# Kernel optimization log

Measured on AMD Instinct MI355X. Metric: run time of the kernel, lower is better.

The kernel has to match this reference:

```python
import jax, jax.numpy as jnp
import numpy as np

N = 20000
E = 320000
IN_F = 256
HEADS = 4
OUT_F = 64
NEG_SLOPE = 0.2


def setup_inputs() -> dict:
    key = jax.random.key(0)
    k1, k2, k3, k4 = jax.random.split(key, 4)
    x = jax.random.normal(k1, (N, IN_F), dtype=jnp.float32)
    edge_index = jax.random.randint(k2, (2, E), 0, N, dtype=jnp.int64)
    # Linear W: [in_features, heads*out_features] (xavier-ish scale)
    W = jax.random.normal(k3, (IN_F, HEADS * OUT_F), dtype=jnp.float32) * (1.0 / np.sqrt(IN_F))
    # attention vector: [1, heads, 2*out_features]
    att = jax.random.normal(k4, (1, HEADS, 2 * OUT_F), dtype=jnp.float32) * 0.1
    b = jnp.zeros((HEADS * OUT_F,), dtype=jnp.float32)
    return {"x": x, "W": W, "att": att, "b": b, "edge_index": edge_index}


def _leaky_relu(v):
    return jnp.where(v > 0, v, NEG_SLOPE * v)


def reference(x, W, att, b, edge_index):
    n = x.shape[0]
    heads = att.shape[1]
    d = att.shape[2] // 2

    # add self loops: edge_index -> [2, E+N]
    loops = jnp.arange(n, dtype=edge_index.dtype)
    src = jnp.concatenate([edge_index[0], loops])
    dst = jnp.concatenate([edge_index[1], loops])

    # projected node features [N, heads, out]
    h = (x @ W).reshape(n, heads, d)

    # attention scores: leaky_relu is elementwise, so the concat-then-dot
    # splits into src/dst halves of `att` -> avoids materializing h_cat.
    a_src = att[0, :, :d]  # [heads, out]
    a_dst = att[0, :, d:]  # [heads, out]
    h_src = h[src]  # [Etot, heads, out]
    scores = (
        jnp.einsum("ehd,hd->eh", _leaky_relu(h_src), a_src)
        + jnp.einsum("ehd,hd->eh", _leaky_relu(h[dst]), a_dst)
    )  # [Etot, heads]

    # NOTE: original module applies softmax over ALL edges (dim=0), not per-dst
    w = jax.nn.softmax(scores, axis=0)  # [Etot, heads]

    # scatter-aggregate weighted src features into dst nodes
    out = jax.ops.segment_sum(h_src * w[:, :, None], dst, num_segments=n)  # [N, heads, out]

    return out.reshape(n, heads * d) + b
```

## Files before the change

kernel.cpp:

```cpp
#include <hip/hip_runtime.h>

#define NN 20000
#define EE 320000
#define TE 340000
#define NEG 0.2f
#define NB_SCORE 1329
#define NB_GEMM 625
#define CAP 96

typedef __attribute__((ext_vector_type(8))) _Float16 half8;
typedef __attribute__((ext_vector_type(4))) _Float16 half4v;
typedef __attribute__((ext_vector_type(4))) float f32x4;

__device__ __forceinline__ float lrelu(float v) { return v > 0.f ? v : NEG * v; }

__global__ __launch_bounds__(256) void k_wsplit(const float* __restrict__ W,
                                                _Float16* __restrict__ Wh, _Float16* __restrict__ Wl) {
    int c = blockIdx.x;
    int k = threadIdx.x;
    float w = W[k * 256 + c];
    _Float16 hi = (_Float16)w;
    _Float16 lo = (_Float16)(w - (float)hi);
    int idx = (k >> 3) * 2048 + c * 8 + (k & 7);
    Wh[idx] = hi;
    Wl[idx] = lo;
}

__global__ __launch_bounds__(256, 4) void k_gemm(const float* __restrict__ x,
                                                 const _Float16* __restrict__ Wh,
                                                 const _Float16* __restrict__ Wl,
                                                 const float* __restrict__ att, _Float16* __restrict__ h16,
                                                 float* __restrict__ Es, float* __restrict__ Ed,
                                                 int* __restrict__ cnt) {
    __shared__ _Float16 xh[32][264];
    __shared__ _Float16 xl[32][264];
    const int tid = threadIdx.x;
    const int r0 = blockIdx.x * 32;

    if (tid < 32) cnt[r0 + tid] = 0;

    const float4* x4 = (const float4*)x;
    #pragma unroll
    for (int i = 0; i < 8; ++i) {
        int slot = tid + i * 256;
        int row = slot >> 6, c4 = slot & 63;
        float4 v = x4[(r0 + row) * 64 + c4];
        _Float16 h0 = (_Float16)v.x, h1 = (_Float16)v.y, h2 = (_Float16)v.z, h3 = (_Float16)v.w;
        half4v hv = {h0, h1, h2, h3};
        half4v lv = {(_Float16)(v.x - (float)h0), (_Float16)(v.y - (float)h1),
                     (_Float16)(v.z - (float)h2), (_Float16)(v.w - (float)h3)};
        *(half4v*)&xh[row][c4 * 4] = hv;
        *(half4v*)&xl[row][c4 * 4] = lv;
    }
    __syncthreads();

    const int lane = tid & 63, wid = tid >> 6;
    const int ch = wid;
    const int grp = lane >> 4, li = lane & 15;

    f32x4 acc[2][4];
    #pragma unroll
    for (int rt = 0; rt < 2; ++rt)
        #pragma unroll
        for (int i = 0; i < 4; ++i) acc[rt][i] = (f32x4){0.f, 0.f, 0.f, 0.f};

    const _Float16* bb_h = Wh + (ch * 64 + li) * 8 + grp * 2048;
    const _Float16* bb_l = Wl + (ch * 64 + li) * 8 + grp * 2048;

    for (int ks = 0; ks < 8; ++ks) {
        half8 ah0 = *(const half8*)&xh[li][ks * 32 + grp * 8];
        half8 al0 = *(const half8*)&xl[li][ks * 32 + grp * 8];
        half8 ah1 = *(const half8*)&xh[16 + li][ks * 32 + grp * 8];
        half8 al1 = *(const half8*)&xl[16 + li][ks * 32 + grp * 8];
        const _Float16* ph = bb_h + ks * 8192;
        const _Float16* pl = bb_l + ks * 8192;
        #pragma unroll
        for (int ct = 0; ct < 4; ++ct) {
            half8 bh = *(const half8*)(ph + ct * 128);
            half8 bl = *(const half8*)(pl + ct * 128);
            acc[0][ct] = __builtin_amdgcn_mfma_f32_16x16x32_f16(ah0, bh, acc[0][ct], 0, 0, 0);
            acc[0][ct] = __builtin_amdgcn_mfma_f32_16x16x32_f16(al0, bh, acc[0][ct], 0, 0, 0);
            acc[0][ct] = __builtin_amdgcn_mfma_f32_16x16x32_f16(ah0, bl, acc[0][ct], 0, 0, 0);
            acc[0][ct] = __builtin_amdgcn_mfma_f32_16x16x32_f16(al0, bl, acc[0][ct], 0, 0, 0);
            acc[1][ct] = __builtin_amdgcn_mfma_f32_16x16x32_f16(ah1, bh, acc[1][ct], 0, 0, 0);
            acc[1][ct] = __builtin_amdgcn_mfma_f32_16x16x32_f16(al1, bh, acc[1][ct], 0, 0, 0);
            acc[1][ct] = __builtin_amdgcn_mfma_f32_16x16x32_f16(ah1, bl, acc[1][ct], 0, 0, 0);
            acc[1][ct] = __builtin_amdgcn_mfma_f32_16x16x32_f16(al1, bl, acc[1][ct], 0, 0, 0);
        }
    }

    float pss[2][4] = {{0.f,0.f,0.f,0.f},{0.f,0.f,0.f,0.f}};
    float psd[2][4] = {{0.f,0.f,0.f,0.f},{0.f,0.f,0.f,0.f}};
    #pragma unroll
    for (int rt = 0; rt < 2; ++rt) {
        #pragma unroll
        for (int ct = 0; ct < 4; ++ct) {
            int cl = ct * 16 + li;
            float avc = att[ch * 128 + cl];
            float dvc = att[ch * 128 + 64 + cl];
            #pragma unroll
            for (int reg = 0; reg < 4; ++reg) {
                float v = acc[rt][ct][reg];
                h16[(r0 + rt * 16 + grp * 4 + reg) * 256 + ch * 64 + cl] = (_Float16)v;
                float l = lrelu(v);
                pss[rt][reg] += l * avc;
                psd[rt][reg] += l * dvc;
            }
        }
    }
    #pragma unroll
    for (int rt = 0; rt < 2; ++rt)
        #pragma unroll
        for (int reg = 0; reg < 4; ++reg) {
            #pragma unroll
            for (int m = 1; m < 16; m <<= 1) {
                pss[rt][reg] += __shfl_xor(pss[rt][reg], m, 64);
                psd[rt][reg] += __shfl_xor(psd[rt][reg], m, 64);
            }
        }
    if (li == 0) {
        #pragma unroll
        for (int rt = 0; rt < 2; ++rt)
            #pragma unroll
            for (int reg = 0; reg < 4; ++reg) {
                int row = r0 + rt * 16 + grp * 4 + reg;
                Es[row * 4 + ch] = expf(pss[rt][reg]);
                Ed[row * 4 + ch] = expf(psd[rt][reg]);
            }
    }
}

__global__ __launch_bounds__(256) void k_fill(const int* __restrict__ es, const int* __restrict__ ed,
                                              const float* __restrict__ Es, const float* __restrict__ Ed,
                                              int* __restrict__ cnt, int* __restrict__ bucket,
                                              float4* __restrict__ psum) {
    __shared__ float4 ls[4];
    int e = blockIdx.x * 256 + threadIdx.x;
    int tid = threadIdx.x, lane = tid & 63, wid = tid >> 6;
    float4 p = {0.f, 0.f, 0.f, 0.f};
    if (e < TE) {
        int si = e < EE ? es[e] : e - EE;
        int di = e < EE ? ed[e] : e - EE;
        int pos = atomicAdd(cnt + di, 1);
        if (pos < CAP) bucket[di * CAP + pos] = si;
        float4 a = ((const float4*)Es)[si];
        float4 d = ((const float4*)Ed)[di];
        p.x = a.x * d.x; p.y = a.y * d.y; p.z = a.z * d.z; p.w = a.w * d.w;
    }
    #pragma unroll
    for (int m = 32; m > 0; m >>= 1) {
        p.x += __shfl_xor(p.x, m, 64);
        p.y += __shfl_xor(p.y, m, 64);
        p.z += __shfl_xor(p.z, m, 64);
        p.w += __shfl_xor(p.w, m, 64);
    }
    if (lane == 0) ls[wid] = p;
    __syncthreads();
    if (tid == 0) {
        float4 t;
        t.x = ls[0].x + ls[1].x + ls[2].x + ls[3].x;
        t.y = ls[0].y + ls[1].y + ls[2].y + ls[3].y;
        t.z = ls[0].z + ls[1].z + ls[2].z + ls[3].z;
        t.w = ls[0].w + ls[1].w + ls[2].w + ls[3].w;
        psum[blockIdx.x] = t;
    }
}

__global__ __launch_bounds__(256) void k_comb(const float4* __restrict__ psum, float* __restrict__ hstat) {
    __shared__ float4 zred[4];
    int tid = threadIdx.x, lane = tid & 63, wid = tid >> 6;
    float4 z = {0.f, 0.f, 0.f, 0.f};
    for (int i = tid; i < NB_SCORE; i += 256) {
        float4 s = psum[i];
        z.x += s.x; z.y += s.y; z.z += s.z; z.w += s.w;
    }
    #pragma unroll
    for (int m = 32; m > 0; m >>= 1) {
        z.x += __shfl_xor(z.x, m, 64);
        z.y += __shfl_xor(z.y, m, 64);
        z.z += __shfl_xor(z.z, m, 64);
        z.w += __shfl_xor(z.w, m, 64);
    }
    if (lane == 0) zred[wid] = z;
    __syncthreads();
    if (tid == 0) {
        float4 t;
        t.x = zred[0].x + zred[1].x + zred[2].x + zred[3].x;
        t.y = zred[0].y + zred[1].y + zred[2].y + zred[3].y;
        t.z = zred[0].z + zred[1].z + zred[2].z + zred[3].z;
        t.w = zred[0].w + zred[1].w + zred[2].w + zred[3].w;
        hstat[0] = 1.0f / t.x; hstat[1] = 1.0f / t.y;
        hstat[2] = 1.0f / t.z; hstat[3] = 1.0f / t.w;
    }
}

__global__ __launch_bounds__(256) void k_gather(const int* __restrict__ cnt, const int* __restrict__ bucket,
                                                const float* __restrict__ Es, const float* __restrict__ Ed,
                                                const _Float16* __restrict__ h16, const float* __restrict__ b,
                                                const float* __restrict__ hstat, float* __restrict__ out) {
    int n = blockIdx.x * 4 + (threadIdx.x >> 6);
    int lane = threadIdx.x & 63;
    int head = lane >> 4;
    int len = cnt[n]; len = len < CAP ? len : CAP;
    const int* bsi = bucket + n * CAP;
    const half4v* h4 = (const half4v*)h16;
    float4 a0 = {0.f, 0.f, 0.f, 0.f}, a1 = a0, a2 = a0, a3 = a0;
    int j = 0;
    for (; j + 7 < len; j += 8) {
        int s0 = bsi[j],     s1 = bsi[j + 1], s2 = bsi[j + 2], s3 = bsi[j + 3];
        int s4 = bsi[j + 4], s5 = bsi[j + 5], s6 = bsi[j + 6], s7 = bsi[j + 7];
        float w0 = Es[s0 * 4 + head], w1 = Es[s1 * 4 + head];
        float w2 = Es[s2 * 4 + head], w3 = Es[s3 * 4 + head];
        float w4 = Es[s4 * 4 + head], w5 = Es[s5 * 4 + head];
        float w6 = Es[s6 * 4 + head], w7 = Es[s7 * 4 + head];
        half4v v0 = h4[s0 * 64 + lane], v1 = h4[s1 * 64 + lane];
        half4v v2 = h4[s2 * 64 + lane], v3 = h4[s3 * 64 + lane];
        half4v v4 = h4[s4 * 64 + lane], v5 = h4[s5 * 64 + lane];
        half4v v6 = h4[s6 * 64 + lane], v7 = h4[s7 * 64 + lane];
        a0.x += w0 * (float)v0.x; a0.y += w0 * (float)v0.y; a0.z += w0 * (float)v0.z; a0.w += w0 * (float)v0.w;
        a1.x += w1 * (float)v1.x; a1.y += w1 * (float)v1.y; a1.z += w1 * (float)v1.z; a1.w += w1 * (float)v1.w;
        a2.x += w2 * (float)v2.x; a2.y += w2 * (float)v2.y; a2.z += w2 * (float)v2.z; a2.w += w2 * (float)v2.w;
        a3.x += w3 * (float)v3.x; a3.y += w3 * (float)v3.y; a3.z += w3 * (float)v3.z; a3.w += w3 * (float)v3.w;
        a0.x += w4 * (float)v4.x; a0.y += w4 * (float)v4.y; a0.z += w4 * (float)v4.z; a0.w += w4 * (float)v4.w;
        a1.x += w5 * (float)v5.x; a1.y += w5 * (float)v5.y; a1.z += w5 * (float)v5.z; a1.w += w5 * (float)v5.w;
        a2.x += w6 * (float)v6.x; a2.y += w6 * (float)v6.y; a2.z += w6 * (float)v6.z; a2.w += w6 * (float)v6.w;
        a3.x += w7 * (float)v7.x; a3.y += w7 * (float)v7.y; a3.z += w7 * (float)v7.z; a3.w += w7 * (float)v7.w;
    }
    for (; j + 3 < len; j += 4) {
        int s0 = bsi[j], s1 = bsi[j + 1], s2 = bsi[j + 2], s3 = bsi[j + 3];
        float w0 = Es[s0 * 4 + head], w1 = Es[s1 * 4 + head];
        float w2 = Es[s2 * 4 + head], w3 = Es[s3 * 4 + head];
        half4v v0 = h4[s0 * 64 + lane], v1 = h4[s1 * 64 + lane];
        half4v v2 = h4[s2 * 64 + lane], v3 = h4[s3 * 64 + lane];
        a0.x += w0 * (float)v0.x; a0.y += w0 * (float)v0.y; a0.z += w0 * (float)v0.z; a0.w += w0 * (float)v0.w;
        a1.x += w1 * (float)v1.x; a1.y += w1 * (float)v1.y; a1.z += w1 * (float)v1.z; a1.w += w1 * (float)v1.w;
        a2.x += w2 * (float)v2.x; a2.y += w2 * (float)v2.y; a2.z += w2 * (float)v2.z; a2.w += w2 * (float)v2.w;
        a3.x += w3 * (float)v3.x; a3.y += w3 * (float)v3.y; a3.z += w3 * (float)v3.z; a3.w += w3 * (float)v3.w;
    }
    for (; j < len; ++j) {
        int s = bsi[j];
        float w = Es[s * 4 + head];
        half4v hv = h4[s * 64 + lane];
        a0.x += w * (float)hv.x; a0.y += w * (float)hv.y; a0.z += w * (float)hv.z; a0.w += w * (float)hv.w;
    }
    float scale = hstat[head] * Ed[n * 4 + head];
    float4 bb = ((const float4*)b)[lane];
    float4 o;
    o.x = bb.x + scale * (a0.x + a1.x + a2.x + a3.x);
    o.y = bb.y + scale * (a0.y + a1.y + a2.y + a3.y);
    o.z = bb.z + scale * (a0.z + a1.z + a2.z + a3.z);
    o.w = bb.w + scale * (a0.w + a1.w + a2.w + a3.w);
    ((float4*)out)[n * 64 + lane] = o;
}

extern "C" void kernel_launch(void* const* d_in, const int* in_sizes, int n_in,
                              void* d_out, int out_size, void* d_ws, size_t ws_size,
                              hipStream_t stream) {
    const float* x   = (const float*)d_in[0];
    const float* W   = (const float*)d_in[1];
    const float* att = (const float*)d_in[2];
    const float* b   = (const float*)d_in[3];
    const int*  eidx = (const int*)d_in[4];
    const int* es = eidx;
    const int* ed = eidx + EE;
    float* out = (float*)d_out;

    float* ws = (float*)d_ws;
    _Float16* h16 = (_Float16*)ws;
    float* Es     = (float*)(h16 + NN * 256);
    float* Ed     = Es + NN * 4;
    int*   cnt    = (int*)(Ed + NN * 4);
    int*   bucket = cnt + NN;
    float4* psum  = (float4*)(bucket + NN * CAP);
    float* hstat  = (float*)(psum + NB_SCORE + 1);
    _Float16* Wh  = (_Float16*)(hstat + 16);
    _Float16* Wl  = Wh + 256 * 256;

    k_wsplit<<<256, 256, 0, stream>>>(W, Wh, Wl);
    k_gemm  <<<NB_GEMM, 256, 0, stream>>>(x, Wh, Wl, att, h16, Es, Ed, cnt);
    k_fill  <<<NB_SCORE, 256, 0, stream>>>(es, ed, Es, Ed, cnt, bucket, psum);
    k_comb  <<<1, 256, 0, stream>>>(psum, hstat);
    k_gather<<<NN / 4, 256, 0, stream>>>(cnt, bucket, Es, Ed, h16, b, hstat, out);
}
```

Baseline: 86.42 us.

## Fuse softmax-normalizer reduction into fill via last-block pattern, shrink bucket indices

Removes the separate single-block combine kernel. The last fill block, found through an atomic done-counter that k_wsplit resets, now sums the per-block partial sums and writes the inverse normalizers. Bucket source indices are stored as 16-bit values, halving bucket traffic in fill and gather, and gather gains a 16-wide unrolled loop for more memory-level parallelism. This saves one kernel launch but adds atomics and fences, and the 16-bit indices only work because N is below 65536.

```diff
diff --git a/kernel.cpp b/kernel.cpp
--- a/kernel.cpp
+++ b/kernel.cpp
@@ -15,7 +15,9 @@
 __device__ __forceinline__ float lrelu(float v) { return v > 0.f ? v : NEG * v; }
 
 __global__ __launch_bounds__(256) void k_wsplit(const float* __restrict__ W,
-                                                _Float16* __restrict__ Wh, _Float16* __restrict__ Wl) {
+                                                _Float16* __restrict__ Wh, _Float16* __restrict__ Wl,
+                                                unsigned* __restrict__ done) {
+    if (blockIdx.x == 0 && threadIdx.x == 0) *done = 0u;
     int c = blockIdx.x;
     int k = threadIdx.x;
     float w = W[k * 256 + c];
@@ -132,9 +134,11 @@
 
 __global__ __launch_bounds__(256) void k_fill(const int* __restrict__ es, const int* __restrict__ ed,
                                               const float* __restrict__ Es, const float* __restrict__ Ed,
-                                              int* __restrict__ cnt, int* __restrict__ bucket,
-                                              float4* __restrict__ psum) {
+                                              int* __restrict__ cnt, unsigned short* __restrict__ bucket,
+                                              float* __restrict__ psumF, unsigned* __restrict__ done,
+                                              float* __restrict__ hstat) {
     __shared__ float4 ls[4];
+    __shared__ int amLast;
     int e = blockIdx.x * 256 + threadIdx.x;
     int tid = threadIdx.x, lane = tid & 63, wid = tid >> 6;
     float4 p = {0.f, 0.f, 0.f, 0.f};
@@ -142,7 +146,7 @@
         int si = e < EE ? es[e] : e - EE;
         int di = e < EE ? ed[e] : e - EE;
         int pos = atomicAdd(cnt + di, 1);
-        if (pos < CAP) bucket[di * CAP + pos] = si;
+        if (pos < CAP) bucket[di * CAP + pos] = (unsigned short)si;
         float4 a = ((const float4*)Es)[si];
         float4 d = ((const float4*)Ed)[di];
         p.x = a.x * d.x; p.y = a.y * d.y; p.z = a.z * d.z; p.w = a.w * d.w;
@@ -162,39 +166,48 @@
         t.y = ls[0].y + ls[1].y + ls[2].y + ls[3].y;
         t.z = ls[0].z + ls[1].z + ls[2].z + ls[3].z;
         t.w = ls[0].w + ls[1].w + ls[2].w + ls[3].w;
-        psum[blockIdx.x] = t;
-    }
-}
-
-__global__ __launch_bounds__(256) void k_comb(const float4* __restrict__ psum, float* __restrict__ hstat) {
-    __shared__ float4 zred[4];
-    int tid = threadIdx.x, lane = tid & 63, wid = tid >> 6;
-    float4 z = {0.f, 0.f, 0.f, 0.f};
-    for (int i = tid; i < NB_SCORE; i += 256) {
-        float4 s = psum[i];
-        z.x += s.x; z.y += s.y; z.z += s.z; z.w += s.w;
-    }
-    #pragma unroll
-    for (int m = 32; m > 0; m >>= 1) {
-        z.x += __shfl_xor(z.x, m, 64);
-        z.y += __shfl_xor(z.y, m, 64);
-        z.z += __shfl_xor(z.z, m, 64);
-        z.w += __shfl_xor(z.w, m, 64);
-    }
-    if (lane == 0) zred[wid] = z;
+        atomicExch(psumF + blockIdx.x * 4 + 0, t.x);
+        atomicExch(psumF + blockIdx.x * 4 + 1, t.y);
+        atomicExch(psumF + blockIdx.x * 4 + 2, t.z);
+        atomicExch(psumF + blockIdx.x * 4 + 3, t.w);
+        __threadfence();
+        unsigned v = atomicAdd(done, 1u);
+        amLast = (v == NB_SCORE - 1);
+    }
     __syncthreads();
-    if (tid == 0) {
-        float4 t;
-        t.x = zred[0].x + zred[1].x + zred[2].x + zred[3].x;
-        t.y = zred[0].y + zred[1].y + zred[2].y + zred[3].y;
-        t.z = zred[0].z + zred[1].z + zred[2].z + zred[3].z;
-        t.w = zred[0].w + zred[1].w + zred[2].w + zred[3].w;
-        hstat[0] = 1.0f / t.x; hstat[1] = 1.0f / t.y;
-        hstat[2] = 1.0f / t.z; hstat[3] = 1.0f / t.w;
-    }
-}
-
-__global__ __launch_bounds__(256) void k_gather(const int* __restrict__ cnt, const int* __restrict__ bucket,
+    if (amLast) {
+        __threadfence();
+        float4 z = {0.f, 0.f, 0.f, 0.f};
+        for (int i = tid; i < NB_SCORE; i += 256) {
+            z.x += atomicAdd(psumF + i * 4 + 0, 0.0f);
+            z.y += atomicAdd(psumF + i * 4 + 1, 0.0f);
+            z.z += atomicAdd(psumF + i * 4 + 2, 0.0f);
+            z.w += atomicAdd(psumF + i * 4 + 3, 0.0f);
+        }
+        #pragma unroll
+        for (int m = 32; m > 0; m >>= 1) {
+            z.x += __shfl_xor(z.x, m, 64);
+            z.y += __shfl_xor(z.y, m, 64);
+            z.z += __shfl_xor(z.z, m, 64);
+            z.w += __shfl_xor(z.w, m, 64);
+        }
+        __syncthreads();
+        if (lane == 0) ls[wid] = z;
+        __syncthreads();
+        if (tid == 0) {
+            float4 t;
+            t.x = ls[0].x + ls[1].x + ls[2].x + ls[3].x;
+            t.y = ls[0].y + ls[1].y + ls[2].y + ls[3].y;
+            t.z = ls[0].z + ls[1].z + ls[2].z + ls[3].z;
+            t.w = ls[0].w + ls[1].w + ls[2].w + ls[3].w;
+            hstat[0] = 1.0f / t.x; hstat[1] = 1.0f / t.y;
+            hstat[2] = 1.0f / t.z; hstat[3] = 1.0f / t.w;
+        }
+    }
+}
+
+__global__ __launch_bounds__(256) void k_gather(const int* __restrict__ cnt,
+                                                const unsigned short* __restrict__ bucket,
                                                 const float* __restrict__ Es, const float* __restrict__ Ed,
                                                 const _Float16* __restrict__ h16, const float* __restrict__ b,
                                                 const float* __restrict__ hstat, float* __restrict__ out) {
@@ -202,10 +215,32 @@
     int lane = threadIdx.x & 63;
     int head = lane >> 4;
     int len = cnt[n]; len = len < CAP ? len : CAP;
-    const int* bsi = bucket + n * CAP;
+    const unsigned short* bsi = bucket + n * CAP;
     const half4v* h4 = (const half4v*)h16;
     float4 a0 = {0.f, 0.f, 0.f, 0.f}, a1 = a0, a2 = a0, a3 = a0;
     int j = 0;
+    for (; j + 15 < len; j += 16) {
+        int s[16];
+        float w[16];
+        #pragma unroll
+        for (int q = 0; q < 16; ++q) s[q] = bsi[j + q];
+        #pragma unroll
+        for (int q = 0; q < 16; ++q) w[q] = Es[s[q] * 4 + head];
+        half4v v[16];
+        #pragma unroll
+        for (int q = 0; q < 16; ++q) v[q] = h4[s[q] * 64 + lane];
+        #pragma unroll
+        for (int q = 0; q < 16; q += 4) {
+            a0.x += w[q] * (float)v[q].x;     a0.y += w[q] * (float)v[q].y;
+            a0.z += w[q] * (float)v[q].z;     a0.w += w[q] * (float)v[q].w;
+            a1.x += w[q+1] * (float)v[q+1].x; a1.y += w[q+1] * (float)v[q+1].y;
+            a1.z += w[q+1] * (float)v[q+1].z; a1.w += w[q+1] * (float)v[q+1].w;
+            a2.x += w[q+2] * (float)v[q+2].x; a2.y += w[q+2] * (float)v[q+2].y;
+            a2.z += w[q+2] * (float)v[q+2].z; a2.w += w[q+2] * (float)v[q+2].w;
+            a3.x += w[q+3] * (float)v[q+3].x; a3.y += w[q+3] * (float)v[q+3].y;
+            a3.z += w[q+3] * (float)v[q+3].z; a3.w += w[q+3] * (float)v[q+3].w;
+        }
+    }
     for (; j + 7 < len; j += 8) {
         int s0 = bsi[j],     s1 = bsi[j + 1], s2 = bsi[j + 2], s3 = bsi[j + 3];
         int s4 = bsi[j + 4], s5 = bsi[j + 5], s6 = bsi[j + 6], s7 = bsi[j + 7];
@@ -270,15 +305,15 @@
     float* Es     = (float*)(h16 + NN * 256);
     float* Ed     = Es + NN * 4;
     int*   cnt    = (int*)(Ed + NN * 4);
-    int*   bucket = cnt + NN;
-    float4* psum  = (float4*)(bucket + NN * CAP);
-    float* hstat  = (float*)(psum + NB_SCORE + 1);
-    _Float16* Wh  = (_Float16*)(hstat + 16);
+    unsigned short* bucket = (unsigned short*)(cnt + NN);
+    float* psumF  = (float*)(bucket + NN * CAP);
+    unsigned* done = (unsigned*)(psumF + NB_SCORE * 4);
+    float* hstat  = (float*)(done + 3);
+    _Float16* Wh  = (_Float16*)(hstat + 12);
     _Float16* Wl  = Wh + 256 * 256;
 
-    k_wsplit<<<256, 256, 0, stream>>>(W, Wh, Wl);
+    k_wsplit<<<256, 256, 0, stream>>>(W, Wh, Wl, done);
     k_gemm  <<<NB_GEMM, 256, 0, stream>>>(x, Wh, Wl, att, h16, Es, Ed, cnt);
-    k_fill  <<<NB_SCORE, 256, 0, stream>>>(es, ed, Es, Ed, cnt, bucket, psum);
-    k_comb  <<<1, 256, 0, stream>>>(psum, hstat);
+    k_fill  <<<NB_SCORE, 256, 0, stream>>>(es, ed, Es, Ed, cnt, bucket, psumF, done, hstat);
     k_gather<<<NN / 4, 256, 0, stream>>>(cnt, bucket, Es, Ed, h16, b, hstat, out);
 }
```

New measurement: 124.2 us. 1.44x slower.
